# Performance work log

Measured on AMD Instinct MI355X. Metric: run time of the kernel, lower is better.

The kernel has to match this reference:

```python
import jax, jax.numpy as jnp
import numpy as np

B, H, W, DIM, HEADS, WS, SHIFT, MLP_RATIO = 32, 56, 56, 256, 8, 7, 3, 4
N = WS * WS                      # tokens per window = 49
NW = (H // WS) * (W // WS)       # windows per image = 64
HEAD_DIM = DIM // HEADS
HIDDEN = DIM * MLP_RATIO


def _rel_index():
    # standard Swin relative position index, shape (N, N), values in [0, (2*WS-1)^2)
    coords = np.stack(np.meshgrid(np.arange(WS), np.arange(WS), indexing='ij')).reshape(2, -1)
    rel = (coords[:, :, None] - coords[:, None, :]).transpose(1, 2, 0)
    rel[:, :, 0] += WS - 1
    rel[:, :, 1] += WS - 1
    rel[:, :, 0] *= 2 * WS - 1
    return rel.sum(-1).astype(np.int32)


def _attn_mask():
    # shifted-window attention mask, shape (NW, N, N), values in {0, -100}
    img = np.zeros((H, W))
    slices = (slice(0, -WS), slice(-WS, -SHIFT), slice(-SHIFT, None))
    cnt = 0
    for hs in slices:
        for ws_ in slices:
            img[hs, ws_] = cnt
            cnt += 1
    mw = img.reshape(H // WS, WS, W // WS, WS).transpose(0, 2, 1, 3).reshape(-1, N)
    diff = mw[:, None, :] - mw[:, :, None]
    return np.where(diff != 0, -100.0, 0.0).astype(np.float32)


def setup_inputs() -> dict:
    key = jax.random.key(0)
    ks = jax.random.split(key, 16)
    s = 0.02
    return {
        'x': jax.random.normal(ks[0], (B, H * W, DIM), jnp.float32),
        'norm1_w': jnp.ones((DIM,), jnp.float32),
        'norm1_b': jnp.zeros((DIM,), jnp.float32),
        'qkv_w': jax.random.normal(ks[1], (3 * DIM, DIM), jnp.float32) * s,
        'qkv_b': jnp.zeros((3 * DIM,), jnp.float32),
        'rpb_table': jax.random.normal(ks[2], ((2 * WS - 1) ** 2, HEADS), jnp.float32) * s,
        'proj_w': jax.random.normal(ks[3], (DIM, DIM), jnp.float32) * s,
        'proj_b': jnp.zeros((DIM,), jnp.float32),
        'norm2_w': jnp.ones((DIM,), jnp.float32),
        'norm2_b': jnp.zeros((DIM,), jnp.float32),
        'fc1_w': jax.random.normal(ks[4], (HIDDEN, DIM), jnp.float32) * s,
        'fc1_b': jnp.zeros((HIDDEN,), jnp.float32),
        'fc2_w': jax.random.normal(ks[5], (DIM, HIDDEN), jnp.float32) * s,
        'fc2_b': jnp.zeros((DIM,), jnp.float32),
        'rel_idx': jnp.asarray(_rel_index()),
        'attn_mask': jnp.asarray(_attn_mask()),
    }


def _ln(t, w, b):
    mu = t.mean(-1, keepdims=True)
    var = ((t - mu) ** 2).mean(-1, keepdims=True)
    return (t - mu) * jax.lax.rsqrt(var + 1e-5) * w + b


def reference(x, norm1_w, norm1_b, qkv_w, qkv_b, rpb_table, proj_w, proj_b,
              norm2_w, norm2_b, fc1_w, fc1_b, fc2_w, fc2_b, rel_idx, attn_mask):
    Bz = x.shape[0]
    shortcut = x
    h = _ln(x, norm1_w, norm1_b).reshape(Bz, H, W, DIM)
    h = jnp.roll(h, (-SHIFT, -SHIFT), axis=(1, 2))                      # cyclic shift
    # window partition -> (Bz*NW, N, C)
    h = h.reshape(Bz, H // WS, WS, W // WS, WS, DIM).transpose(0, 1, 3, 2, 4, 5).reshape(-1, N, DIM)
    qkv = (h @ qkv_w.T + qkv_b).reshape(-1, N, 3, HEADS, HEAD_DIM).transpose(2, 0, 3, 1, 4)
    q, k, v = qkv[0], qkv[1], qkv[2]                                    # (Bz*NW, heads, N, d)
    scale = HEAD_DIM ** -0.5
    attn = jnp.einsum('whnd,whmd->whnm', q * scale, k)
    bias = rpb_table[rel_idx].transpose(2, 0, 1)                        # (heads, N, N)
    attn = attn + bias[None]
    attn = attn.reshape(Bz, NW, HEADS, N, N) + attn_mask[None, :, None]  # shift mask
    attn = jax.nn.softmax(attn.reshape(-1, HEADS, N, N), axis=-1)
    out = jnp.einsum('whnm,whmd->whnd', attn, v).transpose(0, 2, 1, 3).reshape(-1, N, DIM)
    out = out @ proj_w.T + proj_b
    # window reverse + un-shift
    out = out.reshape(Bz, H // WS, W // WS, WS, WS, DIM).transpose(0, 1, 3, 2, 4, 5).reshape(Bz, H, W, DIM)
    out = jnp.roll(out, (SHIFT, SHIFT), axis=(1, 2)).reshape(Bz, H * W, DIM)
    x = shortcut + out
    # residual MLP (pre-LN), exact GELU as in nn.GELU default
    h2 = _ln(x, norm2_w, norm2_b)
    h2 = jax.nn.gelu(h2 @ fc1_w.T + fc1_b, approximate=False)
    return x + (h2 @ fc2_w.T + fc2_b)
```

## Files before the change

kernel.cpp:

```cpp
#include <hip/hip_runtime.h>

typedef unsigned short ushort_t;
typedef __attribute__((ext_vector_type(8))) __bf16 bf16x8;
typedef __attribute__((ext_vector_type(4))) float floatx4;

#define TOKS 100352

__device__ __forceinline__ ushort_t f2bf(float f) {
    union { float f; unsigned u; } a; a.f = f;
    unsigned r = a.u + 0x7fffu + ((a.u >> 16) & 1u);
    return (ushort_t)(r >> 16);
}
__device__ __forceinline__ float bf2f(ushort_t u) {
    union { unsigned v; float f; } a; a.v = ((unsigned)u) << 16; return a.f;
}

__device__ __forceinline__ void async16(const void* g, void* l) {
    __builtin_amdgcn_global_load_lds(
        (const __attribute__((address_space(1))) unsigned int*)g,
        (__attribute__((address_space(3))) unsigned int*)l,
        16, 0, 0);
}

__device__ __forceinline__ int win_to_orig(int t) {
    int b = t / 3136, rr = t - b * 3136;
    int w_ = rr / 49, pos = rr - w_ * 49;
    int wi = w_ >> 3, wj = w_ & 7;
    int ti = pos / 7, tj = pos - ti * 7;
    int h = wi * 7 + ti + 3; if (h >= 56) h -= 56;
    int w = wj * 7 + tj + 3; if (w >= 56) w -= 56;
    return b * 3136 + h * 56 + w;
}

__global__ void convert_kernel(const float* __restrict__ qkv_w, const float* __restrict__ proj_w,
                               const float* __restrict__ fc1_w, const float* __restrict__ fc2_w,
                               const float* __restrict__ rpb, const int* __restrict__ rel_idx,
                               const float* __restrict__ amask,
                               ushort_t* __restrict__ wq, ushort_t* __restrict__ wp,
                               ushort_t* __restrict__ w1, ushort_t* __restrict__ w2,
                               ushort_t* __restrict__ bm) {
    int i = blockIdx.x * 256 + threadIdx.x;
    if (i < 196608) wq[i] = f2bf(qkv_w[i]);
    if (i < 65536)  wp[i] = f2bf(proj_w[i]);
    if (i < 262144) { w1[i] = f2bf(fc1_w[i]); w2[i] = f2bf(fc2_w[i]); }
    if (i < 1229312) {
        int wh = i / 2401, ij = i - wh * 2401;
        int head = wh & 7, wimg = wh >> 3;
        bm[i] = f2bf(rpb[rel_idx[ij] * 8 + head] + amask[wimg * 2401 + ij]);
    }
}

__global__ __launch_bounds__(256) void ln_kernel(const float* __restrict__ xin,
                                                 const float* __restrict__ gw,
                                                 const float* __restrict__ gb,
                                                 ushort_t* __restrict__ outb) {
    const int wid = threadIdx.x >> 6, lane = threadIdx.x & 63;
    const int t_out = blockIdx.x * 4 + wid;
    const int t_in = win_to_orig(t_out);
    const float4* src = (const float4*)(xin + (long)t_in * 256);
    float4 v = src[lane];
    float s  = v.x + v.y + v.z + v.w;
    float s2 = v.x*v.x + v.y*v.y + v.z*v.z + v.w*v.w;
    #pragma unroll
    for (int d = 32; d >= 1; d >>= 1) { s += __shfl_xor(s, d, 64); s2 += __shfl_xor(s2, d, 64); }
    float mu  = s * 0.00390625f;
    float var = s2 * 0.00390625f - mu * mu;
    float ry  = rsqrtf(var + 1e-5f);
    float4 w4 = ((const float4*)gw)[lane], b4 = ((const float4*)gb)[lane];
    unsigned long long p =
          (unsigned long long)f2bf((v.x - mu) * ry * w4.x + b4.x)
        | ((unsigned long long)f2bf((v.y - mu) * ry * w4.y + b4.y) << 16)
        | ((unsigned long long)f2bf((v.z - mu) * ry * w4.z + b4.z) << 32)
        | ((unsigned long long)f2bf((v.w - mu) * ry * w4.w + b4.w) << 48);
    ((unsigned long long*)(outb + (long)t_out * 256))[lane] = p;
}

template <int MODE, int N_LD, int KD, int CT>
__global__ __launch_bounds__(256, 2) void gemm_kernel(const ushort_t* __restrict__ A,
                                                      const ushort_t* __restrict__ Bw,
                                                      const float* __restrict__ bias,
                                                      void* __restrict__ outp,
                                                      const ushort_t* __restrict__ x1w,
                                                      int rowOff) {
    __shared__ __align__(16) ushort_t As[128 * 32];
    __shared__ __align__(16) ushort_t Bs[128 * 32];
    const int tid = threadIdx.x;
    const int lane = tid & 63;
    const int wid = tid >> 6;
    const int wm = wid & 1, wn = wid >> 1;
    const int l15 = lane & 15, quad = lane >> 4;
    const int v = blockIdx.x;
    const int j = v >> 3;
    const long tileM = (long)((j / CT) * 8 + (v & 7)) * 128;
    const long tileN = (long)(j % CT) * 128;

    floatx4 acc[4][4];
    #pragma unroll
    for (int i = 0; i < 4; i++)
        #pragma unroll
        for (int jj = 0; jj < 4; jj++) acc[i][jj] = {0.f, 0.f, 0.f, 0.f};

    const int o1 = tid * 16;
    const int r1 = o1 >> 6, c1 = (o1 & 63) >> 1;
    const ushort_t* Ar1 = A + (tileM + r1) * KD + c1;
    const ushort_t* Ar2 = A + (tileM + r1 + 64) * KD + c1;
    const ushort_t* Br1 = Bw + (tileN + r1) * KD + c1;
    const ushort_t* Br2 = Bw + (tileN + r1 + 64) * KD + c1;
    ushort_t* Ad1 = &As[o1 >> 1];
    ushort_t* Ad2 = &As[(o1 >> 1) + 2048];
    ushort_t* Bd1 = &Bs[o1 >> 1];
    ushort_t* Bd2 = &Bs[(o1 >> 1) + 2048];

    for (int k0 = 0; k0 < KD; k0 += 32) {
        async16(Ar1 + k0, Ad1);
        async16(Ar2 + k0, Ad2);
        async16(Br1 + k0, Bd1);
        async16(Br2 + k0, Bd2);
        __syncthreads();
        bf16x8 af[4], bfr[4];
        #pragma unroll
        for (int mi = 0; mi < 4; mi++)
            af[mi] = *(const bf16x8*)&As[(wm * 64 + mi * 16 + l15) * 32 + quad * 8];
        #pragma unroll
        for (int nj = 0; nj < 4; nj++)
            bfr[nj] = *(const bf16x8*)&Bs[(wn * 64 + nj * 16 + l15) * 32 + quad * 8];
        #pragma unroll
        for (int mi = 0; mi < 4; mi++)
            #pragma unroll
            for (int nj = 0; nj < 4; nj++)
                acc[mi][nj] = __builtin_amdgcn_mfma_f32_16x16x32_bf16(af[mi], bfr[nj], acc[mi][nj], 0, 0, 0);
        __syncthreads();
    }

    #pragma unroll
    for (int mi = 0; mi < 4; mi++)
      #pragma unroll
      for (int nj = 0; nj < 4; nj++)
        #pragma unroll
        for (int r = 0; r < 4; r++) {
            long row = tileM + wm * 64 + mi * 16 + quad * 4 + r;
            long col = tileN + wn * 64 + nj * 16 + l15;
            float val = acc[mi][nj][r] + bias[col];
            if (MODE == 0) {
                ((ushort_t*)outp)[row * N_LD + col] = f2bf(val);
            } else if (MODE == 2) {
                float g = 0.5f * val * (1.f + erff(val * 0.70710678118654752f));
                ((ushort_t*)outp)[row * N_LD + col] = f2bf(g);
            } else {
                float res = bf2f(x1w[row * 256 + col]);
                int orig = win_to_orig((int)row + rowOff);
                ((float*)outp)[(long)orig * 256 + col] = val + res;
            }
        }
}

__global__ __launch_bounds__(256, 2) void proj_ln_kernel(
        const ushort_t* __restrict__ A, const ushort_t* __restrict__ Bw,
        const float* __restrict__ pb, const float* __restrict__ x_res,
        const float* __restrict__ n2w, const float* __restrict__ n2b,
        ushort_t* __restrict__ x1w, ushort_t* __restrict__ h2out) {
    __shared__ __align__(16) ushort_t As[64 * 32];
    __shared__ __align__(16) ushort_t Bs[256 * 32];
    __shared__ float red_s[4][64];
    __shared__ float red_q[4][64];
    const int tid = threadIdx.x, lane = tid & 63, wid = tid >> 6;
    const int l15 = lane & 15, quad = lane >> 4;
    const long tileM = (long)blockIdx.x * 64;

    floatx4 acc[4][4];
    #pragma unroll
    for (int i = 0; i < 4; i++)
        #pragma unroll
        for (int j = 0; j < 4; j++) acc[i][j] = {0.f, 0.f, 0.f, 0.f};

    const int oA = tid * 16;
    const int rA = oA >> 6, cA = (oA & 63) >> 1;
    const ushort_t* Ap = A + (tileM + rA) * 256 + cA;
    ushort_t* Ad = &As[oA >> 1];

    for (int k0 = 0; k0 < 256; k0 += 32) {
        async16(Ap + k0, Ad);
        #pragma unroll
        for (int ch = 0; ch < 4; ch++) {
            int o = ch * 4096 + oA;
            async16(Bw + (o >> 6) * 256 + ((o & 63) >> 1) + k0, &Bs[o >> 1]);
        }
        __syncthreads();
        bf16x8 af[4], bfr[4];
        #pragma unroll
        for (int mi = 0; mi < 4; mi++)
            af[mi] = *(const bf16x8*)&As[(mi * 16 + l15) * 32 + quad * 8];
        #pragma unroll
        for (int nj = 0; nj < 4; nj++)
            bfr[nj] = *(const bf16x8*)&Bs[(wid * 64 + nj * 16 + l15) * 32 + quad * 8];
        #pragma unroll
        for (int mi = 0; mi < 4; mi++)
            #pragma unroll
            for (int nj = 0; nj < 4; nj++)
                acc[mi][nj] = __builtin_amdgcn_mfma_f32_16x16x32_bf16(af[mi], bfr[nj], acc[mi][nj], 0, 0, 0);
        __syncthreads();
    }

    #pragma unroll
    for (int mi = 0; mi < 4; mi++)
      #pragma unroll
      for (int r = 0; r < 4; r++) {
        int iloc = mi * 16 + quad * 4 + r;
        int orig = win_to_orig((int)tileM + iloc);
        float s = 0.f, q = 0.f;
        #pragma unroll
        for (int nj = 0; nj < 4; nj++) {
            int col = wid * 64 + nj * 16 + l15;
            float val = acc[mi][nj][r] + pb[col] + x_res[(long)orig * 256 + col];
            x1w[(tileM + iloc) * 256 + col] = f2bf(val);
            acc[mi][nj][r] = val;
            s += val; q += val * val;
        }
        #pragma unroll
        for (int d = 1; d < 16; d <<= 1) { s += __shfl_xor(s, d, 64); q += __shfl_xor(q, d, 64); }
        if (l15 == 0) { red_s[wid][iloc] = s; red_q[wid][iloc] = q; }
      }
    __syncthreads();
    #pragma unroll
    for (int mi = 0; mi < 4; mi++)
      #pragma unroll
      for (int r = 0; r < 4; r++) {
        int iloc = mi * 16 + quad * 4 + r;
        float s = red_s[0][iloc] + red_s[1][iloc] + red_s[2][iloc] + red_s[3][iloc];
        float q = red_q[0][iloc] + red_q[1][iloc] + red_q[2][iloc] + red_q[3][iloc];
        float mu = s * 0.00390625f;
        float var = q * 0.00390625f - mu * mu;
        float rstd = rsqrtf(var + 1e-5f);
        #pragma unroll
        for (int nj = 0; nj < 4; nj++) {
            int col = wid * 64 + nj * 16 + l15;
            float val = acc[mi][nj][r];
            h2out[(tileM + iloc) * 256 + col] = f2bf((val - mu) * rstd * n2w[col] + n2b[col]);
        }
      }
}

__global__ __launch_bounds__(256) void attn_kernel(const ushort_t* __restrict__ qkv,
                                                   const ushort_t* __restrict__ bm,
                                                   ushort_t* __restrict__ attnout) {
    __shared__ __align__(16) ushort_t lds[4 * 5832];
    const int tid = threadIdx.x, lane = tid & 63, wid = tid >> 6;
    ushort_t* Pl = &lds[wid * 5832];
    ushort_t* Vt = Pl + 49 * 72;
    const int whid = blockIdx.x * 4 + wid;
    const int win = whid >> 3, head = whid & 7;
    const int l15 = lane & 15, quad = lane >> 4;
    const long base = (long)win * 49 * 768;
    const ushort_t* bmw = bm + (long)((win & 63) * 8 + head) * 2401;

    bf16x8 qf[4], kf[4];
    #pragma unroll
    for (int t4 = 0; t4 < 4; t4++) {
        int tok = t4 * 16 + l15; if (tok > 48) tok = 48;
        const ushort_t* p = qkv + base + (long)tok * 768 + head * 32 + quad * 8;
        qf[t4] = *(const bf16x8*)p;
        kf[t4] = *(const bf16x8*)(p + 256);
    }

    floatx4 S[4][4];
    #pragma unroll
    for (int mi = 0; mi < 4; mi++)
        #pragma unroll
        for (int nj = 0; nj < 4; nj++) {
            floatx4 z = {0.f, 0.f, 0.f, 0.f};
            S[mi][nj] = __builtin_amdgcn_mfma_f32_16x16x32_bf16(qf[mi], kf[nj], z, 0, 0, 0);
        }

    {
        int jl = lane;
        int jc = jl < 49 ? jl : 48;
        const uint4* vsrc = (const uint4*)(qkv + base + (long)jc * 768 + 512 + head * 32);
        uint4 vz; vz.x = vz.y = vz.z = vz.w = 0u;
        #pragma unroll
        for (int q4 = 0; q4 < 4; q4++) {
            uint4 vv = (jl < 49) ? vsrc[q4] : vz;
            int db = q4 * 8;
            Vt[(db+0)*72 + jl] = (ushort_t)vv.x;  Vt[(db+1)*72 + jl] = (ushort_t)(vv.x >> 16);
            Vt[(db+2)*72 + jl] = (ushort_t)vv.y;  Vt[(db+3)*72 + jl] = (ushort_t)(vv.y >> 16);
            Vt[(db+4)*72 + jl] = (ushort_t)vv.z;  Vt[(db+5)*72 + jl] = (ushort_t)(vv.z >> 16);
            Vt[(db+6)*72 + jl] = (ushort_t)vv.w;  Vt[(db+7)*72 + jl] = (ushort_t)(vv.w >> 16);
        }
    }

    const float scale = 0.17677669529663687f;
    #pragma unroll
    for (int mi = 0; mi < 4; mi++)
      #pragma unroll
      for (int nj = 0; nj < 4; nj++)
        #pragma unroll
        for (int r = 0; r < 4; r++) {
            int i = mi * 16 + quad * 4 + r;
            int jj = nj * 16 + l15;
            float s = -1e30f;
            if (i < 49 && jj < 49) s = S[mi][nj][r] * scale + bf2f(bmw[i * 49 + jj]);
            S[mi][nj][r] = s;
        }

    float rinv[4][4];
    #pragma unroll
    for (int mi = 0; mi < 4; mi++)
      #pragma unroll
      for (int r = 0; r < 4; r++) {
          float m = fmaxf(fmaxf(S[mi][0][r], S[mi][1][r]), fmaxf(S[mi][2][r], S[mi][3][r]));
          #pragma unroll
          for (int d = 1; d < 16; d <<= 1) m = fmaxf(m, __shfl_xor(m, d, 64));
          float e[4], sum = 0.f;
          #pragma unroll
          for (int nj = 0; nj < 4; nj++) { e[nj] = __expf(S[mi][nj][r] - m); sum += e[nj]; }
          #pragma unroll
          for (int d = 1; d < 16; d <<= 1) sum += __shfl_xor(sum, d, 64);
          rinv[mi][r] = 1.f / sum;
          int i = mi * 16 + quad * 4 + r;
          if (i < 49) {
              #pragma unroll
              for (int nj = 0; nj < 4; nj++) Pl[i * 72 + (nj * 16 + l15)] = f2bf(e[nj]);
          }
      }

    __syncthreads();

    floatx4 O[4][2];
    #pragma unroll
    for (int mi = 0; mi < 4; mi++) { O[mi][0] = {0.f,0.f,0.f,0.f}; O[mi][1] = {0.f,0.f,0.f,0.f}; }
    #pragma unroll
    for (int kc = 0; kc < 2; kc++) {
        bf16x8 pf[4], vf[2];
        #pragma unroll
        for (int mi = 0; mi < 4; mi++) {
            int pr = mi * 16 + l15; if (pr > 48) pr = 48;
            pf[mi] = *(const bf16x8*)&Pl[pr * 72 + kc * 32 + quad * 8];
        }
        #pragma unroll
        for (int n2 = 0; n2 < 2; n2++)
            vf[n2] = *(const bf16x8*)&Vt[(n2 * 16 + l15) * 72 + kc * 32 + quad * 8];
        #pragma unroll
        for (int mi = 0; mi < 4; mi++)
            #pragma unroll
            for (int n2 = 0; n2 < 2; n2++)
                O[mi][n2] = __builtin_amdgcn_mfma_f32_16x16x32_bf16(pf[mi], vf[n2], O[mi][n2], 0, 0, 0);
    }

    #pragma unroll
    for (int mi = 0; mi < 4; mi++)
      #pragma unroll
      for (int n2 = 0; n2 < 2; n2++)
        #pragma unroll
        for (int r = 0; r < 4; r++) {
            int i = mi * 16 + quad * 4 + r;
            if (i < 49) {
                long orow = ((long)win * 49 + i) * 256 + head * 32 + n2 * 16 + l15;
                attnout[orow] = f2bf(O[mi][n2][r] * rinv[mi][r]);
            }
        }
}

extern "C" void kernel_launch(void* const* d_in, const int* in_sizes, int n_in,
                              void* d_out, int out_size, void* d_ws, size_t ws_size,
                              hipStream_t stream) {
    const float* x      = (const float*)d_in[0];
    const float* n1w    = (const float*)d_in[1];
    const float* n1b    = (const float*)d_in[2];
    const float* qkv_w  = (const float*)d_in[3];
    const float* qkv_b  = (const float*)d_in[4];
    const float* rpb    = (const float*)d_in[5];
    const float* proj_w = (const float*)d_in[6];
    const float* proj_b = (const float*)d_in[7];
    const float* n2w    = (const float*)d_in[8];
    const float* n2b    = (const float*)d_in[9];
    const float* fc1_w  = (const float*)d_in[10];
    const float* fc1_b  = (const float*)d_in[11];
    const float* fc2_w  = (const float*)d_in[12];
    const float* fc2_b  = (const float*)d_in[13];
    const int*   rel_idx= (const int*)d_in[14];
    const float* amask  = (const float*)d_in[15];

    char* ws = (char*)d_ws;
    ushort_t* wq   = (ushort_t*)(ws + 0);
    ushort_t* wp   = (ushort_t*)(ws + 393216);
    ushort_t* w1   = (ushort_t*)(ws + 524288);
    ushort_t* w2   = (ushort_t*)(ws + 1048576);
    ushort_t* hwin = (ushort_t*)(ws + 1572864);
    ushort_t* qkvb = (ushort_t*)(ws + 52953088);
    ushort_t* h2   = (ushort_t*)(ws + 104333312);
    ushort_t* x1w  = (ushort_t*)(ws + 155713536);
    ushort_t* h3   = hwin;
    ushort_t* bm = (ushort_t*)d_out;

    convert_kernel<<<4803, 256, 0, stream>>>(qkv_w, proj_w, fc1_w, fc2_w, rpb, rel_idx,
                                             amask, wq, wp, w1, w2, bm);
    ln_kernel<<<TOKS / 4, 256, 0, stream>>>(x, n1w, n1b, hwin);
    gemm_kernel<0, 768, 256, 6><<<4704, 256, 0, stream>>>(hwin, wq, qkv_b, qkvb, nullptr, 0);
    attn_kernel<<<4096, 256, 0, stream>>>(qkvb, bm, hwin);
    proj_ln_kernel<<<1568, 256, 0, stream>>>(hwin, wp, proj_b, x, n2w, n2b, x1w, h2);
    for (int c = 0; c < 2; c++) {
        gemm_kernel<2, 1024, 256, 8><<<3136, 256, 0, stream>>>(
            h2 + (long)c * 50176 * 256, w1, fc1_b, h3, nullptr, 0);
        gemm_kernel<4, 256, 1024, 2><<<784, 256, 0, stream>>>(
            h3, w2, fc2_b, (float*)d_out, x1w + (long)c * 50176 * 256, c * 50176);
    }
    (void)in_sizes; (void)n_in; (void)out_size; (void)ws_size;
}
```

Measured before the change: 655.9 us.

## Prefold scale into Q weights and preload bias-mask as MFMA accumulator

The softmax scale is folded into the Q rows of the QKV weight and bias during conversion. The relative-position bias plus shift mask is precomputed as fp32 in the MFMA accumulator fragment layout, with -1e30 padding, and loaded directly as the initial S accumulator. This removes the per-element scale/bias/mask fixup and the scattered bf16 bias loads. V loads are issued before the QK MFMAs and the block barrier is dropped, since each wave uses private LDS. The cost is a larger fp32 bias table (8 MB) and more conversion work.

```diff
diff --git a/kernel.cpp b/kernel.cpp
--- a/kernel.cpp
+++ b/kernel.cpp
@@ -35,18 +35,26 @@
 __global__ void convert_kernel(const float* __restrict__ qkv_w, const float* __restrict__ proj_w,
                                const float* __restrict__ fc1_w, const float* __restrict__ fc2_w,
                                const float* __restrict__ rpb, const int* __restrict__ rel_idx,
-                               const float* __restrict__ amask,
+                               const float* __restrict__ amask, const float* __restrict__ qkv_b,
                                ushort_t* __restrict__ wq, ushort_t* __restrict__ wp,
                                ushort_t* __restrict__ w1, ushort_t* __restrict__ w2,
-                               ushort_t* __restrict__ bm) {
+                               float* __restrict__ bmF, float* __restrict__ qb2) {
+    const float scale = 0.17677669529663687f;
     int i = blockIdx.x * 256 + threadIdx.x;
-    if (i < 196608) wq[i] = f2bf(qkv_w[i]);
+    if (i < 196608) { float v = qkv_w[i]; wq[i] = f2bf(i < 65536 ? v * scale : v); }
     if (i < 65536)  wp[i] = f2bf(proj_w[i]);
     if (i < 262144) { w1[i] = f2bf(fc1_w[i]); w2[i] = f2bf(fc2_w[i]); }
-    if (i < 1229312) {
-        int wh = i / 2401, ij = i - wh * 2401;
+    if (i < 768)    qb2[i] = qkv_b[i] * (i < 256 ? scale : 1.f);
+    if (i < 2097152) {
+        int r = i & 3, lane = (i >> 2) & 63, t = (i >> 8) & 15, wh = i >> 12;
         int head = wh & 7, wimg = wh >> 3;
-        bm[i] = f2bf(rpb[rel_idx[ij] * 8 + head] + amask[wimg * 2401 + ij]);
+        int mi = t >> 2, nj = t & 3;
+        int quad = lane >> 4, l15 = lane & 15;
+        int ii = mi * 16 + quad * 4 + r, jj = nj * 16 + l15;
+        float val = -1e30f;
+        if (ii < 49 && jj < 49)
+            val = rpb[rel_idx[ii * 49 + jj] * 8 + head] + amask[wimg * 2401 + ii * 49 + jj];
+        bmF[i] = val;
     }
 }
 
@@ -241,7 +249,7 @@
 }
 
 __global__ __launch_bounds__(256) void attn_kernel(const ushort_t* __restrict__ qkv,
-                                                   const ushort_t* __restrict__ bm,
+                                                   const float* __restrict__ bmF,
                                                    ushort_t* __restrict__ attnout) {
     __shared__ __align__(16) ushort_t lds[4 * 5832];
     const int tid = threadIdx.x, lane = tid & 63, wid = tid >> 6;
@@ -251,7 +259,15 @@
     const int win = whid >> 3, head = whid & 7;
     const int l15 = lane & 15, quad = lane >> 4;
     const long base = (long)win * 49 * 768;
-    const ushort_t* bmw = bm + (long)((win & 63) * 8 + head) * 2401;
+
+    const floatx4* bmc = (const floatx4*)bmF
+                       + ((long)((win & 63) * 8 + head) * 16) * 64 + lane;
+    floatx4 S[4][4];
+    #pragma unroll
+    for (int mi = 0; mi < 4; mi++)
+        #pragma unroll
+        for (int nj = 0; nj < 4; nj++)
+            S[mi][nj] = bmc[(mi * 4 + nj) * 64];
 
     bf16x8 qf[4], kf[4];
     #pragma unroll
@@ -262,44 +278,29 @@
         kf[t4] = *(const bf16x8*)(p + 256);
     }
 
-    floatx4 S[4][4];
-    #pragma unroll
-    for (int mi = 0; mi < 4; mi++)
-        #pragma unroll
-        for (int nj = 0; nj < 4; nj++) {
-            floatx4 z = {0.f, 0.f, 0.f, 0.f};
-            S[mi][nj] = __builtin_amdgcn_mfma_f32_16x16x32_bf16(qf[mi], kf[nj], z, 0, 0, 0);
-        }
-
-    {
-        int jl = lane;
-        int jc = jl < 49 ? jl : 48;
-        const uint4* vsrc = (const uint4*)(qkv + base + (long)jc * 768 + 512 + head * 32);
-        uint4 vz; vz.x = vz.y = vz.z = vz.w = 0u;
-        #pragma unroll
-        for (int q4 = 0; q4 < 4; q4++) {
-            uint4 vv = (jl < 49) ? vsrc[q4] : vz;
-            int db = q4 * 8;
-            Vt[(db+0)*72 + jl] = (ushort_t)vv.x;  Vt[(db+1)*72 + jl] = (ushort_t)(vv.x >> 16);
-            Vt[(db+2)*72 + jl] = (ushort_t)vv.y;  Vt[(db+3)*72 + jl] = (ushort_t)(vv.y >> 16);
-            Vt[(db+4)*72 + jl] = (ushort_t)vv.z;  Vt[(db+5)*72 + jl] = (ushort_t)(vv.z >> 16);
-            Vt[(db+6)*72 + jl] = (ushort_t)vv.w;  Vt[(db+7)*72 + jl] = (ushort_t)(vv.w >> 16);
-        }
-    }
-
-    const float scale = 0.17677669529663687f;
-    #pragma unroll
-    for (int mi = 0; mi < 4; mi++)
-      #pragma unroll
-      for (int nj = 0; nj < 4; nj++)
-        #pragma unroll
-        for (int r = 0; r < 4; r++) {
-            int i = mi * 16 + quad * 4 + r;
-            int jj = nj * 16 + l15;
-            float s = -1e30f;
-            if (i < 49 && jj < 49) s = S[mi][nj][r] * scale + bf2f(bmw[i * 49 + jj]);
-            S[mi][nj][r] = s;
-        }
+    const int jl = lane;
+    const int jc = jl < 49 ? jl : 48;
+    const uint4* vsrc = (const uint4*)(qkv + base + (long)jc * 768 + 512 + head * 32);
+    uint4 vz; vz.x = vz.y = vz.z = vz.w = 0u;
+    uint4 vv[4];
+    #pragma unroll
+    for (int q4 = 0; q4 < 4; q4++) vv[q4] = (jl < 49) ? vsrc[q4] : vz;
+
+    #pragma unroll
+    for (int mi = 0; mi < 4; mi++)
+        #pragma unroll
+        for (int nj = 0; nj < 4; nj++)
+            S[mi][nj] = __builtin_amdgcn_mfma_f32_16x16x32_bf16(qf[mi], kf[nj], S[mi][nj], 0, 0, 0);
+
+    #pragma unroll
+    for (int q4 = 0; q4 < 4; q4++) {
+        int db = q4 * 8;
+        uint4 v4 = vv[q4];
+        Vt[(db+0)*72 + jl] = (ushort_t)v4.x;  Vt[(db+1)*72 + jl] = (ushort_t)(v4.x >> 16);
+        Vt[(db+2)*72 + jl] = (ushort_t)v4.y;  Vt[(db+3)*72 + jl] = (ushort_t)(v4.y >> 16);
+        Vt[(db+4)*72 + jl] = (ushort_t)v4.z;  Vt[(db+5)*72 + jl] = (ushort_t)(v4.z >> 16);
+        Vt[(db+6)*72 + jl] = (ushort_t)v4.w;  Vt[(db+7)*72 + jl] = (ushort_t)(v4.w >> 16);
+    }
 
     float rinv[4][4];
     #pragma unroll
@@ -322,7 +323,6 @@
           }
       }
 
-    __syncthreads();
 
     floatx4 O[4][2];
     #pragma unroll
@@ -389,13 +389,14 @@
     ushort_t* h2   = (ushort_t*)(ws + 104333312);
     ushort_t* x1w  = (ushort_t*)(ws + 155713536);
     ushort_t* h3   = hwin;
-    ushort_t* bm = (ushort_t*)d_out;
-
-    convert_kernel<<<4803, 256, 0, stream>>>(qkv_w, proj_w, fc1_w, fc2_w, rpb, rel_idx,
-                                             amask, wq, wp, w1, w2, bm);
+    float* bmF = (float*)d_out;
+    float* qb2 = (float*)((char*)d_out + 8388608);
+
+    convert_kernel<<<8192, 256, 0, stream>>>(qkv_w, proj_w, fc1_w, fc2_w, rpb, rel_idx,
+                                             amask, qkv_b, wq, wp, w1, w2, bmF, qb2);
     ln_kernel<<<TOKS / 4, 256, 0, stream>>>(x, n1w, n1b, hwin);
-    gemm_kernel<0, 768, 256, 6><<<4704, 256, 0, stream>>>(hwin, wq, qkv_b, qkvb, nullptr, 0);
-    attn_kernel<<<4096, 256, 0, stream>>>(qkvb, bm, hwin);
+    gemm_kernel<0, 768, 256, 6><<<4704, 256, 0, stream>>>(hwin, wq, qb2, qkvb, nullptr, 0);
+    attn_kernel<<<4096, 256, 0, stream>>>(qkvb, bmF, hwin);
     proj_ln_kernel<<<1568, 256, 0, stream>>>(hwin, wp, proj_b, x, n2w, n2b, x1w, h2);
     for (int c = 0; c < 2; c++) {
         gemm_kernel<2, 1024, 256, 8><<<3136, 256, 0, stream>>>(
```

Result: faster. 640.3 us (-2.4%).
